# Kernel optimization log

Measured on AMD Instinct MI355X. Metric: run time of the kernel, lower is better.

## Reference

```python
import jax, jax.numpy as jnp
import numpy as np

B, T, I, H = 512, 512, 8, 256


def setup_inputs() -> dict:
    key = jax.random.key(0)
    ks = jax.random.split(key, 4)
    x = jax.random.normal(ks[0], (B, T, I), dtype=jnp.float32)
    W_ih = jax.random.normal(ks[1], (3 * H, I), dtype=jnp.float32) * 0.1
    W_hh = jax.random.normal(ks[2], (3 * H, H), dtype=jnp.float32) * 0.05
    b_ih = jnp.zeros((3 * H,), dtype=jnp.float32)
    b_hh = jnp.zeros((3 * H,), dtype=jnp.float32)
    W_lin = jax.random.normal(ks[3], (1, H), dtype=jnp.float32) * 0.05
    b_lin = jnp.zeros((1,), dtype=jnp.float32)
    return {"x": x, "W_ih": W_ih, "W_hh": W_hh, "b_ih": b_ih,
            "b_hh": b_hh, "W_lin": W_lin, "b_lin": b_lin,
            "pred_length": T}


def reference(x, W_ih, W_hh, b_ih, b_hh, W_lin, b_lin, pred_length):
    # GRU (pred_type='full'): emit lin_usage(h_t) at every timestep.
    Hd = W_hh.shape[1]

    def step(h, x_t):
        gi = x_t @ W_ih.T + b_ih          # [B, 3H]
        gh = h @ W_hh.T + b_hh            # [B, 3H]
        i_r, i_z, i_n = jnp.split(gi, 3, axis=-1)
        h_r, h_z, h_n = jnp.split(gh, 3, axis=-1)
        r = jax.nn.sigmoid(i_r + h_r)
        z = jax.nn.sigmoid(i_z + h_z)
        n = jnp.tanh(i_n + r * h_n)
        h_new = (1.0 - z) * n + z * h
        pred = h_new @ W_lin.T + b_lin    # [B, 1]
        return h_new, pred

    h0 = jnp.zeros((x.shape[0], Hd), dtype=x.dtype)
    _, preds = jax.lax.scan(step, h0, jnp.swapaxes(x, 0, 1))  # preds: [T, B, 1]
    return jnp.swapaxes(preds, 0, 1)                          # [B, T, 1]
```

## Files before the change

### kernel.cpp

```cpp
#include <hip/hip_runtime.h>

#define TT 512
#define II 8
#define HH 256
#define ST 296
#define RR 8
#define NB 64

typedef _Float16 h4_t  __attribute__((ext_vector_type(4)));
typedef _Float16 h8_t  __attribute__((ext_vector_type(8)));
typedef float    f32x4 __attribute__((ext_vector_type(4)));

__device__ inline h8_t cvt8(const float* __restrict__ p, float s) {
    h8_t r;
#pragma unroll
    for (int i = 0; i < 8; ++i) r[i] = (_Float16)(p[i] * s);
    return r;
}

__global__ void __launch_bounds__(512, 2) gru_kernel(
    const float* __restrict__ x,    const float* __restrict__ W_ih,
    const float* __restrict__ W_hh, const float* __restrict__ b_ih,
    const float* __restrict__ b_hh, const float* __restrict__ W_lin,
    const float* __restrict__ b_lin, float* __restrict__ out)
{
    __shared__ _Float16 hbuf[2][16][ST];
    __shared__ h8_t wz1buf[8 * 8 * 64];
    __shared__ h8_t wn1buf[8 * 8 * 64];

    const int tid  = threadIdx.x;
    const int w    = tid >> 6;
    const int lane = tid & 63;
    const int q    = lane >> 4;
    const int r15  = lane & 15;
    const int row0 = blockIdx.x * RR;

    const float sRZ = -1.44269504088896340736f;
    const float sN  =  2.88539008177792681472f;

    const int c0 = w * 32 + r15;
    const int c1 = c0 + 16;

    h8_t wfR0[8], wfZ0[8], wfN0[8], wfR1[8];
#pragma unroll
    for (int s = 0; s < 8; ++s) {
        const int k0 = s * 32 + q * 8;
        wfR0[s] = cvt8(W_hh + (size_t)(c0)       * HH + k0, sRZ);
        wfZ0[s] = cvt8(W_hh + (size_t)(256 + c0) * HH + k0, sRZ);
        wfN0[s] = cvt8(W_hh + (size_t)(512 + c0) * HH + k0, sN);
        wfR1[s] = cvt8(W_hh + (size_t)(c1)       * HH + k0, sRZ);
        wz1buf[(w * 8 + s) * 64 + lane] = cvt8(W_hh + (size_t)(256 + c1) * HH + k0, sRZ);
        wn1buf[(w * 8 + s) * 64 + lane] = cvt8(W_hh + (size_t)(512 + c1) * HH + k0, sN);
    }
    h4_t xfR[2], xfZ[2], xfN[2];
#pragma unroll
    for (int g = 0; g < 2; ++g) {
        const int cR = g ? c1 : c0;
#pragma unroll
        for (int j = 0; j < 4; ++j) {
            const int kp = q * 4 + j;
            float vR = 0.f, vZ = 0.f, vN = 0.f;
            if (kp < 8) {
                vR = W_ih[(cR)       * II + kp] * sRZ;
                vZ = W_ih[(256 + cR) * II + kp] * sRZ;
                vN = W_ih[(512 + cR) * II + kp] * sN;
            } else if (kp == 8) {
                vR = (b_ih[cR]       + b_hh[cR])       * sRZ;
                vZ = (b_ih[256 + cR] + b_hh[256 + cR]) * sRZ;
                vN = b_ih[512 + cR] * sN;
            }
            xfR[g][j] = (_Float16)vR; xfZ[g][j] = (_Float16)vZ; xfN[g][j] = (_Float16)vN;
        }
    }
    const bool hi = (lane >= 32);
    const float bhnp = (hi ? b_hh[512 + c1] : b_hh[512 + c0]) * sN;
    const float blin = b_lin[0];
    const float wl0 = W_lin[lane * 4 + 0], wl1 = W_lin[lane * 4 + 1];
    const float wl2 = W_lin[lane * 4 + 2], wl3 = W_lin[lane * 4 + 3];

    for (int i = tid; i < 2 * 16 * ST; i += 512) (&hbuf[0][0][0])[i] = (_Float16)0.f;
    __syncthreads();
    if (tid < 32) hbuf[tid >> 4][tid & 15][264] = (_Float16)1.f;
    if (tid < 64) {
        const int rr_ = tid >> 3, ii = tid & 7;
        const _Float16 xh = (_Float16)x[((size_t)(row0 + rr_) * TT + 0) * II + ii];
        hbuf[0][rr_][256 + ii]     = xh;
        hbuf[0][rr_ + 8][256 + ii] = xh;
    }
    __syncthreads();

    const h8_t* __restrict__ wz_lane = &wz1buf[w * 8 * 64 + lane];
    const h8_t* __restrict__ wn_lane = &wn1buf[w * 8 * 64 + lane];

    f32x4 hreg = {0.f, 0.f, 0.f, 0.f};
    const f32x4 z4 = {0.f, 0.f, 0.f, 0.f};

    const int rb   = (q & 1) * 4;
    const int colp = hi ? c1 : c0;

    for (int t = 0; t < TT; ++t) {
        const int cur = t & 1, nxt = cur ^ 1;

        float xv = 0.f;
        {
            const int tn = (t + 1 < TT) ? t + 1 : TT - 1;
            if (lane < II) xv = x[((size_t)(row0 + w) * TT + tn) * II + lane];
        }

        const _Float16* hb = &hbuf[cur][r15][0];
        const h4_t a2 = *(const h4_t*)(hb + 256 + q * 4);
        f32x4 accR0 = __builtin_amdgcn_mfma_f32_16x16x16f16(a2, xfR[0], z4, 0, 0, 0);
        f32x4 accZ0 = __builtin_amdgcn_mfma_f32_16x16x16f16(a2, xfZ[0], z4, 0, 0, 0);
        f32x4 gin0  = __builtin_amdgcn_mfma_f32_16x16x16f16(a2, xfN[0], z4, 0, 0, 0);
        f32x4 accR1 = __builtin_amdgcn_mfma_f32_16x16x16f16(a2, xfR[1], z4, 0, 0, 0);
        f32x4 accZ1 = __builtin_amdgcn_mfma_f32_16x16x16f16(a2, xfZ[1], z4, 0, 0, 0);
        f32x4 gin1  = __builtin_amdgcn_mfma_f32_16x16x16f16(a2, xfN[1], z4, 0, 0, 0);
        f32x4 accN0 = z4, accN1 = z4;
#pragma unroll
        for (int s = 0; s < 8; ++s) {
            const h8_t a  = *(const h8_t*)(hb + s * 32 + q * 8);
            const h8_t wz = wz_lane[s * 64];
            const h8_t wn = wn_lane[s * 64];
            accR0 = __builtin_amdgcn_mfma_f32_16x16x32_f16(a, wfR0[s], accR0, 0, 0, 0);
            accZ0 = __builtin_amdgcn_mfma_f32_16x16x32_f16(a, wfZ0[s], accZ0, 0, 0, 0);
            accN0 = __builtin_amdgcn_mfma_f32_16x16x32_f16(a, wfN0[s], accN0, 0, 0, 0);
            accR1 = __builtin_amdgcn_mfma_f32_16x16x32_f16(a, wfR1[s], accR1, 0, 0, 0);
            accZ1 = __builtin_amdgcn_mfma_f32_16x16x32_f16(a, wz,     accZ1, 0, 0, 0);
            accN1 = __builtin_amdgcn_mfma_f32_16x16x32_f16(a, wn,     accN1, 0, 0, 0);
        }

        if (t > 0) {
            const h4_t hv4 = *(const h4_t*)&hbuf[cur][w][lane * 4];
            float s0 = (float)hv4[0] * wl0 + (float)hv4[1] * wl1
                     + (float)hv4[2] * wl2 + (float)hv4[3] * wl3;
#pragma unroll
            for (int m = 32; m >= 1; m >>= 1) s0 += __shfl_xor(s0, m, 64);
            if (lane == 0) out[(size_t)(row0 + w) * TT + (t - 1)] = s0 + blin;
        }

        _Float16* hw = &hbuf[nxt][rb][colp];
#pragma unroll
        for (int j = 0; j < 4; ++j) {
            const float vR = hi ? accR1[j] : accR0[j];
            const float vZ = hi ? accZ1[j] : accZ0[j];
            const float vN = hi ? accN1[j] : accN0[j];
            const float vG = hi ? gin1[j]  : gin0[j];
            const float rr = __builtin_amdgcn_rcpf(1.f + __builtin_amdgcn_exp2f(vR));
            const float zz = __builtin_amdgcn_rcpf(1.f + __builtin_amdgcn_exp2f(vZ));
            const float u  = vG + rr * (vN + bhnp);
            const float nn = 1.f - 2.f * __builtin_amdgcn_rcpf(1.f + __builtin_amdgcn_exp2f(u));
            const float hv = nn + zz * (hreg[j] - nn);
            hreg[j] = hv;
            const _Float16 hh = (_Float16)hv;
            hw[j * ST]          = hh;
            hw[j * ST + 8 * ST] = hh;
        }
        if (lane < II) {
            const _Float16 xh = (_Float16)xv;
            hbuf[nxt][w][256 + lane]     = xh;
            hbuf[nxt][w + 8][256 + lane] = xh;
        }

        __syncthreads();
    }

    {
        const h4_t hv4 = *(const h4_t*)&hbuf[TT & 1][w][lane * 4];
        float s0 = (float)hv4[0] * wl0 + (float)hv4[1] * wl1
                 + (float)hv4[2] * wl2 + (float)hv4[3] * wl3;
#pragma unroll
        for (int m = 32; m >= 1; m >>= 1) s0 += __shfl_xor(s0, m, 64);
        if (lane == 0) out[(size_t)(row0 + w) * TT + (TT - 1)] = s0 + blin;
    }
}

extern "C" void kernel_launch(void* const* d_in, const int* in_sizes, int n_in,
                              void* d_out, int out_size, void* d_ws, size_t ws_size,
                              hipStream_t stream) {
    const float* x     = (const float*)d_in[0];
    const float* W_ih  = (const float*)d_in[1];
    const float* W_hh  = (const float*)d_in[2];
    const float* b_ih  = (const float*)d_in[3];
    const float* b_hh  = (const float*)d_in[4];
    const float* W_lin = (const float*)d_in[5];
    const float* b_lin = (const float*)d_in[6];
    float* out = (float*)d_out;
    gru_kernel<<<NB, 512, 0, stream>>>(x, W_ih, W_hh, b_ih, b_hh, W_lin, b_lin, out);
}
```

Before: 888.2 us.

## Stage x in 16-step LDS windows and batch prediction stores per 64 steps

Replaces the per-timestep global load of the next x row with a coalesced prefetch of 16 timesteps per block, converted to fp16 into a double-buffered LDS staging area. Bias and padding inputs for the small MFMA are built in registers instead of being read from hbuf. Per-step scalar output stores are buffered in LDS and written out coalesced every 64 steps. This takes global memory latency and tiny scattered stores off the serial recurrence, at the cost of extra LDS and some conditional logic on boundary steps.

```diff
diff --git a/kernel.cpp b/kernel.cpp
--- a/kernel.cpp
+++ b/kernel.cpp
@@ -6,9 +6,11 @@
 #define ST 296
 #define RR 8
 #define NB 64
+#define XSR 136
 
 typedef _Float16 h4_t  __attribute__((ext_vector_type(4)));
 typedef _Float16 h8_t  __attribute__((ext_vector_type(8)));
+typedef float    f32x2 __attribute__((ext_vector_type(2)));
 typedef float    f32x4 __attribute__((ext_vector_type(4)));
 
 __device__ inline h8_t cvt8(const float* __restrict__ p, float s) {
@@ -27,6 +29,8 @@
     __shared__ _Float16 hbuf[2][16][ST];
     __shared__ h8_t wz1buf[8 * 8 * 64];
     __shared__ h8_t wn1buf[8 * 8 * 64];
+    __shared__ _Float16 xstage[2][RR][XSR];
+    __shared__ float predbuf[2][RR][64];
 
     const int tid  = threadIdx.x;
     const int w    = tid >> 6;
@@ -78,14 +82,15 @@
     const float wl0 = W_lin[lane * 4 + 0], wl1 = W_lin[lane * 4 + 1];
     const float wl2 = W_lin[lane * 4 + 2], wl3 = W_lin[lane * 4 + 3];
 
+    const h4_t bias4 = {(_Float16)1.f, (_Float16)0.f, (_Float16)0.f, (_Float16)0.f};
+    const h4_t zero4 = {(_Float16)0.f, (_Float16)0.f, (_Float16)0.f, (_Float16)0.f};
+
     for (int i = tid; i < 2 * 16 * ST; i += 512) (&hbuf[0][0][0])[i] = (_Float16)0.f;
-    __syncthreads();
-    if (tid < 32) hbuf[tid >> 4][tid & 15][264] = (_Float16)1.f;
-    if (tid < 64) {
-        const int rr_ = tid >> 3, ii = tid & 7;
-        const _Float16 xh = (_Float16)x[((size_t)(row0 + rr_) * TT + 0) * II + ii];
-        hbuf[0][rr_][256 + ii]     = xh;
-        hbuf[0][rr_ + 8][256 + ii] = xh;
+    {
+        const int rr_ = tid >> 6, f2 = (tid & 63) * 2;
+        const f32x2 v = *(const f32x2*)(x + (size_t)(row0 + rr_) * TT * II + f2);
+        xstage[0][rr_][f2]     = (_Float16)v[0];
+        xstage[0][rr_][f2 + 1] = (_Float16)v[1];
     }
     __syncthreads();
 
@@ -98,17 +103,20 @@
     const int rb   = (q & 1) * 4;
     const int colp = hi ? c1 : c0;
 
+    f32x2 xpre = {0.f, 0.f};
+    const int xrow = tid >> 6, xf2 = (tid & 63) * 2;
+
     for (int t = 0; t < TT; ++t) {
         const int cur = t & 1, nxt = cur ^ 1;
-
-        float xv = 0.f;
-        {
-            const int tn = (t + 1 < TT) ? t + 1 : TT - 1;
-            if (lane < II) xv = x[((size_t)(row0 + w) * TT + tn) * II + lane];
+        const int win = (t >> 4) & 1;
+
+        if ((t & 15) == 0 && t + 16 < TT) {
+            xpre = *(const f32x2*)(x + ((size_t)(row0 + xrow) * TT + (t + 16)) * II + xf2);
         }
 
         const _Float16* hb = &hbuf[cur][r15][0];
-        const h4_t a2 = *(const h4_t*)(hb + 256 + q * 4);
+        const h4_t xa = *(const h4_t*)&xstage[win][r15 & 7][(t & 15) * 8 + (q & 1) * 4];
+        const h4_t a2 = (q < 2) ? xa : ((q == 2) ? bias4 : zero4);
         f32x4 accR0 = __builtin_amdgcn_mfma_f32_16x16x16f16(a2, xfR[0], z4, 0, 0, 0);
         f32x4 accZ0 = __builtin_amdgcn_mfma_f32_16x16x16f16(a2, xfZ[0], z4, 0, 0, 0);
         f32x4 gin0  = __builtin_amdgcn_mfma_f32_16x16x16f16(a2, xfN[0], z4, 0, 0, 0);
@@ -135,7 +143,7 @@
                      + (float)hv4[2] * wl2 + (float)hv4[3] * wl3;
 #pragma unroll
             for (int m = 32; m >= 1; m >>= 1) s0 += __shfl_xor(s0, m, 64);
-            if (lane == 0) out[(size_t)(row0 + w) * TT + (t - 1)] = s0 + blin;
+            if (lane == 0) predbuf[((t - 1) >> 6) & 1][w][(t - 1) & 63] = s0 + blin;
         }
 
         _Float16* hw = &hbuf[nxt][rb][colp];
@@ -155,13 +163,20 @@
             hw[j * ST]          = hh;
             hw[j * ST + 8 * ST] = hh;
         }
-        if (lane < II) {
-            const _Float16 xh = (_Float16)xv;
-            hbuf[nxt][w][256 + lane]     = xh;
-            hbuf[nxt][w + 8][256 + lane] = xh;
+
+        if ((t & 15) == 15 && t + 1 < TT) {
+            _Float16* xd = &xstage[win ^ 1][xrow][xf2];
+            xd[0] = (_Float16)xpre[0];
+            xd[1] = (_Float16)xpre[1];
         }
 
         __syncthreads();
+
+        if ((t & 63) == 0 && t > 0) {
+            const int pb = ((t >> 6) & 1) ^ 1;
+            out[(size_t)(row0 + (tid >> 6)) * TT + (t - 64) + (tid & 63)] =
+                predbuf[pb][tid >> 6][tid & 63];
+        }
     }
 
     {
@@ -170,8 +185,11 @@
                  + (float)hv4[2] * wl2 + (float)hv4[3] * wl3;
 #pragma unroll
         for (int m = 32; m >= 1; m >>= 1) s0 += __shfl_xor(s0, m, 64);
-        if (lane == 0) out[(size_t)(row0 + w) * TT + (TT - 1)] = s0 + blin;
-    }
+        if (lane == 0) predbuf[1][w][63] = s0 + blin;
+    }
+    __syncthreads();
+    out[(size_t)(row0 + (tid >> 6)) * TT + 448 + (tid & 63)] =
+        predbuf[1][tid >> 6][tid & 63];
 }
 
 extern "C" void kernel_launch(void* const* d_in, const int* in_sizes, int n_in,
```

New measurement: 886.5 us. About the same (-0.2%).
